# Performance work log

Measured on AMD Instinct MI355X. Metric: run time of the kernel, lower is better.

## Reference

```python
import jax, jax.numpy as jnp
import numpy as np

DIM = 128
H = 8
HD = DIM // H
NL = 6
DFF = 2048
EPS = 1e-5
S2S_STEPS = 6


def _ln(x, g, b):
    m = jnp.mean(x, -1, keepdims=True)
    v = jnp.mean(jnp.square(x - m), -1, keepdims=True)
    return (x - m) / jnp.sqrt(v + EPS) * g + b


def _lstm_step(x, h, c, wih, whh, bih, bhh):
    # torch LSTM gate order: i, f, g, o
    gates = x @ wih.T + bih + h @ whh.T + bhh
    i, f, g, o = jnp.split(gates, 4, axis=-1)
    c = jax.nn.sigmoid(f) * c + jax.nn.sigmoid(i) * jnp.tanh(g)
    h = jax.nn.sigmoid(o) * jnp.tanh(c)
    return h, c


def setup_inputs() -> dict:
    key = jax.random.key(0)
    ks = iter(jax.random.split(key, 16))
    n = lambda shape: jax.random.normal(next(ks), shape, jnp.float32) * 0.02
    inp = {
        "data": jax.random.normal(next(ks), (64, 256, 3), jnp.float32),
        "lin0_w": n((DIM, 3)), "lin0_b": jnp.zeros((DIM,), jnp.float32),
        "attn_in_w": n((NL, 3 * DIM, DIM)), "attn_in_b": jnp.zeros((NL, 3 * DIM), jnp.float32),
        "attn_out_w": n((NL, DIM, DIM)), "attn_out_b": jnp.zeros((NL, DIM), jnp.float32),
        "ln1_g": jnp.ones((NL, DIM), jnp.float32), "ln1_b": jnp.zeros((NL, DIM), jnp.float32),
        "ff_w1": n((NL, DFF, DIM)), "ff_b1": jnp.zeros((NL, DFF), jnp.float32),
        "ff_w2": n((NL, DIM, DFF)), "ff_b2": jnp.zeros((NL, DIM), jnp.float32),
        "ln2_g": jnp.ones((NL, DIM), jnp.float32), "ln2_b": jnp.zeros((NL, DIM), jnp.float32),
        "s2s_wih": n((4 * DIM, 2 * DIM)), "s2s_whh": n((4 * DIM, DIM)),
        "s2s_bih": jnp.zeros((4 * DIM,), jnp.float32), "s2s_bhh": jnp.zeros((4 * DIM,), jnp.float32),
        "mem_wih": n((4 * DIM, 2 * DIM)), "mem_whh": n((4 * DIM, DIM)),
        "mem_bih": jnp.zeros((4 * DIM,), jnp.float32), "mem_bhh": jnp.zeros((4 * DIM,), jnp.float32),
        "lin1_w": n((DIM, DIM)), "lin1_b": jnp.zeros((DIM,), jnp.float32),
        "lin3_w": n((1, DIM)), "lin3_b": jnp.zeros((1,), jnp.float32),
    }
    return inp


def reference(data, lin0_w, lin0_b, attn_in_w, attn_in_b, attn_out_w, attn_out_b,
              ln1_g, ln1_b, ff_w1, ff_b1, ff_w2, ff_b2, ln2_g, ln2_b,
              s2s_wih, s2s_whh, s2s_bih, s2s_bhh,
              mem_wih, mem_whh, mem_bih, mem_bhh,
              lin1_w, lin1_b, lin3_w, lin3_b):
    x = jax.nn.relu(data @ lin0_w.T + lin0_b)  # [S=64, B=256, D]
    S, B, _ = x.shape
    # torch TransformerEncoder with batch_first=False: attention over axis 0,
    # axis 1 is the transformer batch. Post-norm layers (norm_first=False), relu FFN.
    for l in range(NL):
        qkv = x @ attn_in_w[l].T + attn_in_b[l]
        q, k, v = jnp.split(qkv, 3, axis=-1)
        q = q.reshape(S, B, H, HD)
        k = k.reshape(S, B, H, HD)
        v = v.reshape(S, B, H, HD)
        scores = jnp.einsum('sbhd,tbhd->bhst', q, k) / np.float32(np.sqrt(HD))
        attn = jax.nn.softmax(scores, axis=-1)
        ao = jnp.einsum('bhst,tbhd->sbhd', attn, v).reshape(S, B, DIM)
        x = _ln(x + ao @ attn_out_w[l].T + attn_out_b[l], ln1_g[l], ln1_b[l])
        ff = jax.nn.relu(x @ ff_w1[l].T + ff_b1[l]) @ ff_w2[l].T + ff_b2[l]
        x = _ln(x + ff, ln2_g[l], ln2_b[l])
    # Set2Set pooling: bidxs assign segment = axis-0 index for each block of
    # num_atoms consecutive rows of flatten(out,0,1), i.e. pool over axis 1.
    q_star = jnp.zeros((S, 2 * DIM), x.dtype)
    h = jnp.zeros((S, DIM), x.dtype)
    c = jnp.zeros((S, DIM), x.dtype)
    for _ in range(S2S_STEPS):
        h, c = _lstm_step(q_star, h, c, s2s_wih, s2s_whh, s2s_bih, s2s_bhh)
        e = jnp.einsum('bnd,bd->bn', x, h)          # [S, num_atoms]
        a = jax.nn.softmax(e, axis=-1)              # segment softmax (uniform segs)
        r = jnp.einsum('bn,bnd->bd', a, x)          # segment weighted sum
        q_star = jnp.concatenate([h, r], axis=-1)   # [S, 2D]
    # memory LSTM: seq_len 1, zero initial state (states=None branch)
    hx = jnp.zeros((S, DIM), x.dtype)
    cx = jnp.zeros((S, DIM), x.dtype)
    hx, cx = _lstm_step(q_star, hx, cx, mem_wih, mem_whh, mem_bih, mem_bhh)
    o = jax.nn.relu(hx @ lin1_w.T + lin1_b)
    v_out = (o @ lin3_w.T + lin3_b)[None]  # [1, S, 1]
    return v_out, hx[None], cx[None]
```

## Files before the change

### kernel.cpp

```cpp
#include <hip/hip_runtime.h>
#include <math.h>


typedef _Float16 __attribute__((ext_vector_type(8))) f16x8;
typedef __attribute__((ext_vector_type(4))) float f32x4;
typedef _Float16 __attribute__((ext_vector_type(2))) h16x2;

__device__ __forceinline__ unsigned short f2h(float f) {
  union { _Float16 h; unsigned short s; } x; x.h = (_Float16)f; return x.s;
}
__device__ __forceinline__ float h2f(unsigned short u) {
  union { unsigned short s; _Float16 h; } x; x.s = u; return (float)x.h;
}
__device__ __forceinline__ unsigned packh(float a, float b) {
  return (unsigned)f2h(a) | ((unsigned)f2h(b) << 16);
}
__device__ __forceinline__ float hlo(unsigned u) {
  union { unsigned short s; _Float16 h; } x; x.s = (unsigned short)(u & 0xffff);
  return (float)x.h;
}
__device__ __forceinline__ float hhi(unsigned u) {
  union { unsigned short s; _Float16 h; } x; x.s = (unsigned short)(u >> 16);
  return (float)x.h;
}
__device__ __forceinline__ float fdot2u(unsigned a, unsigned b, float c) {
#if __has_builtin(__builtin_amdgcn_fdot2)
  union U { unsigned u; h16x2 h; };
  U x, y; x.u = a; y.u = b;
  return __builtin_amdgcn_fdot2(x.h, y.h, c, false);
#else
  return c + hlo(a) * hlo(b) + hhi(a) * hhi(b);
#endif
}
__device__ __forceinline__ float sigf(float x) { return 1.f / (1.f + expf(-x)); }

__device__ __forceinline__ void gl2lds16(const void* g, void* l) {
  __builtin_amdgcn_global_load_lds(
      (const __attribute__((address_space(1))) unsigned int*)g,
      (__attribute__((address_space(3))) unsigned int*)l, 16, 0, 0);
}

__global__ __launch_bounds__(256) void convw_kernel(
    const float* __restrict__ aiw, const float* __restrict__ aow,
    const float* __restrict__ w1, const float* __restrict__ w2,
    const float* __restrict__ wih, const float* __restrict__ whh,
    const float* __restrict__ mwih,
    unsigned short* __restrict__ o0, unsigned short* __restrict__ o1,
    unsigned short* __restrict__ o2, unsigned short* __restrict__ o3,
    unsigned short* __restrict__ o4, unsigned short* __restrict__ o5,
    unsigned short* __restrict__ o6) {
  int i = blockIdx.x * 256 + threadIdx.x;
  if (i < 294912) {
    o0[i] = f2h(aiw[i]);
  } else if (i < 393216) {
    int j = i - 294912; o1[j] = f2h(aow[j]);
  } else if (i < 1966080) {
    int j = i - 393216; o2[j] = f2h(w1[j]);
  } else if (i < 3538944) {
    int j = i - 1966080; o3[j] = f2h(w2[j]);
  } else if (i < 3670016) {
    int j = i - 3538944; o4[j] = f2h(wih[j]);
  } else if (i < 3735552) {
    int j = i - 3670016; o5[j] = f2h(whh[j]);
  } else {
    int j = i - 3735552; o6[j] = f2h(mwih[j]);
  }
}

__global__ __launch_bounds__(256) void lin0_kernel(
    const float* __restrict__ data, const float* __restrict__ w,
    const float* __restrict__ b, float* __restrict__ x,
    unsigned short* __restrict__ xb) {
  int i = blockIdx.x * 256 + threadIdx.x;
  int n = i >> 7, d = i & 127;
  float v = b[d] + data[n * 3 + 0] * w[d * 3 + 0]
                 + data[n * 3 + 1] * w[d * 3 + 1]
                 + data[n * 3 + 2] * w[d * 3 + 2];
  v = fmaxf(v, 0.0f);
  x[i] = v;
  xb[i] = f2h(v);
}

__global__ __launch_bounds__(512) void layer_kernel(
    const unsigned short* __restrict__ xbg,
    const unsigned short* __restrict__ wqkv, const float* __restrict__ bqkv,
    const unsigned short* __restrict__ wout, const float* __restrict__ bout,
    const float* __restrict__ ln1g, const float* __restrict__ ln1b,
    const unsigned short* __restrict__ w1, const float* __restrict__ b1,
    const unsigned short* __restrict__ w2, const float* __restrict__ b2,
    const float* __restrict__ ln2g, const float* __restrict__ ln2b,
    float* __restrict__ xio, unsigned short* __restrict__ xbo) {
  __shared__ __align__(16) unsigned short Xs[64 * 128];
  __shared__ __align__(16) unsigned short Ws[256 * 128];
  __shared__ __align__(16) unsigned short U1[128 * 128];
  __shared__ __align__(16) unsigned short U2[128 * 128];
  __shared__ __align__(16) uint4 zchunk;
  __shared__ float psum[8][64], psq[8][64];
  __shared__ float2 stats[64];

  unsigned short* Qs = U1;
  unsigned short* Ks2 = U1 + 8192;
  unsigned short* VT = U2;
  unsigned short* AOs = U2 + 8192;
  unsigned short* Hs = U2;

  int tid = threadIdx.x, w = tid >> 6, lane = tid & 63;
  int b = blockIdx.x;
  int r4 = lane >> 4, cs = lane & 15;
  int fr = lane & 15, fq = lane >> 4;

  if (tid == 0) zchunk = make_uint4(0u, 0u, 0u, 0u);

#pragma unroll
  for (int i = 0; i < 2; i++) {
    int issue = w * 2 + i;
    int row = issue * 4 + r4;
    int g = cs ^ (row & 7);
    gl2lds16(xbg + (size_t)(row * 256 + b) * 128 + g * 8,
             (char*)Xs + issue * 1024);
  }
#pragma unroll
  for (int i = 0; i < 8; i++) {
    int issue = w * 8 + i;
    int row = issue * 4 + r4;
    int g = cs ^ (row & 7);
    gl2lds16(wqkv + (size_t)row * 128 + g * 8, (char*)Ws + issue * 1024);
  }
  __syncthreads();

  f16x8 xfragA[4][4];
#pragma unroll
  for (int ks = 0; ks < 4; ks++)
#pragma unroll
    for (int mi = 0; mi < 4; mi++) {
      int row = mi * 16 + fr;
      int kq = (ks * 4 + fq) ^ (row & 7);
      xfragA[ks][mi] = *(const f16x8*)(Xs + row * 128 + kq * 8);
    }

  {
    f32x4 acc[4][2];
#pragma unroll
    for (int i = 0; i < 4; i++)
#pragma unroll
      for (int j = 0; j < 2; j++) acc[i][j] = (f32x4){0.f, 0.f, 0.f, 0.f};
#pragma unroll
    for (int ks = 0; ks < 4; ks++) {
      f16x8 bf[2];
#pragma unroll
      for (int ni = 0; ni < 2; ni++) {
        int wr = (w * 2 + ni) * 16 + fr;
        int kq = (ks * 4 + fq) ^ (wr & 7);
        bf[ni] = *(const f16x8*)(Ws + wr * 128 + kq * 8);
      }
#pragma unroll
      for (int mi = 0; mi < 4; mi++)
#pragma unroll
        for (int ni = 0; ni < 2; ni++)
          acc[mi][ni] = __builtin_amdgcn_mfma_f32_16x16x32_f16(
              xfragA[ks][mi], bf[ni], acc[mi][ni], 0, 0, 0);
    }
#pragma unroll
    for (int ni = 0; ni < 2; ni++) {
      int c = (w * 2 + ni) * 16 + fr;
      float bv = bqkv[c];
      unsigned short* dst = (c < 128) ? Qs : Ks2;
      int cc = c & 127;
#pragma unroll
      for (int mi = 0; mi < 4; mi++)
#pragma unroll
        for (int r = 0; r < 4; r++) {
          int row = mi * 16 + fq * 4 + r;
          dst[row * 128 + (((cc >> 3) ^ (row & 7)) << 3) + (cc & 7)] =
              f2h(acc[mi][ni][r] + bv);
        }
    }
  }
  __syncthreads();

#pragma unroll
  for (int i = 0; i < 4; i++) {
    int issue = w * 4 + i;
    int row = issue * 4 + r4;
    int g = cs ^ (row & 7);
    gl2lds16(wqkv + (size_t)(256 + row) * 128 + g * 8, (char*)Ws + issue * 1024);
  }
  __syncthreads();

  {
    f32x4 acc[4];
#pragma unroll
    for (int i = 0; i < 4; i++) acc[i] = (f32x4){0.f, 0.f, 0.f, 0.f};
#pragma unroll
    for (int ks = 0; ks < 4; ks++) {
      f16x8 bf;
      {
        int wr = w * 16 + fr;
        int kq = (ks * 4 + fq) ^ (wr & 7);
        bf = *(const f16x8*)(Ws + wr * 128 + kq * 8);
      }
#pragma unroll
      for (int mi = 0; mi < 4; mi++)
        acc[mi] = __builtin_amdgcn_mfma_f32_16x16x32_f16(xfragA[ks][mi], bf,
                                                         acc[mi], 0, 0, 0);
    }
    int f = w * 16 + fr;
    float bv = bqkv[256 + f];
#pragma unroll
    for (int mi = 0; mi < 4; mi++)
#pragma unroll
      for (int r = 0; r < 4; r++) {
        int srow = mi * 16 + fq * 4 + r;
        VT[f * 64 + (((srow >> 3) ^ (f & 7)) << 3) + (srow & 7)] =
            f2h(acc[mi][r] + bv);
      }
  }
  __syncthreads();

  {
    int h = w;
    unsigned short* Pb = Ws + w * 4096;
    f32x4 sc[4][4];
#pragma unroll
    for (int i = 0; i < 4; i++)
#pragma unroll
      for (int j = 0; j < 4; j++) sc[i][j] = (f32x4){0.f, 0.f, 0.f, 0.f};
    {
      f16x8 af[4], bf[4];
#pragma unroll
      for (int mi = 0; mi < 4; mi++) {
        int row = mi * 16 + fr;
        const unsigned short* pa =
            (fq < 2) ? (Qs + row * 128 + (((h * 2 + fq) ^ (row & 7)) << 3))
                     : (const unsigned short*)&zchunk;
        af[mi] = *(const f16x8*)pa;
      }
#pragma unroll
      for (int ti = 0; ti < 4; ti++) {
        int trow = ti * 16 + fr;
        const unsigned short* pb =
            (fq < 2) ? (Ks2 + trow * 128 + (((h * 2 + fq) ^ (trow & 7)) << 3))
                     : (const unsigned short*)&zchunk;
        bf[ti] = *(const f16x8*)pb;
      }
#pragma unroll
      for (int mi = 0; mi < 4; mi++)
#pragma unroll
        for (int ti = 0; ti < 4; ti++)
          sc[mi][ti] = __builtin_amdgcn_mfma_f32_16x16x32_f16(
              af[mi], bf[ti], sc[mi][ti], 0, 0, 0);
    }
#pragma unroll
    for (int mi = 0; mi < 4; mi++) {
#pragma unroll
      for (int r = 0; r < 4; r++) {
        float m = -1e30f;
#pragma unroll
        for (int ti = 0; ti < 4; ti++) m = fmaxf(m, sc[mi][ti][r]);
        m = fmaxf(m, __shfl_xor(m, 1, 64));
        m = fmaxf(m, __shfl_xor(m, 2, 64));
        m = fmaxf(m, __shfl_xor(m, 4, 64));
        m = fmaxf(m, __shfl_xor(m, 8, 64));
        m *= 0.25f;
        float ss = 0.f;
#pragma unroll
        for (int ti = 0; ti < 4; ti++) {
          float p = expf(sc[mi][ti][r] * 0.25f - m);
          sc[mi][ti][r] = p;
          ss += p;
        }
        ss += __shfl_xor(ss, 1, 64);
        ss += __shfl_xor(ss, 2, 64);
        ss += __shfl_xor(ss, 4, 64);
        ss += __shfl_xor(ss, 8, 64);
        float inv = 1.f / ss;
        int prow = mi * 16 + fq * 4 + r;
#pragma unroll
        for (int ti = 0; ti < 4; ti++) {
          int t = ti * 16 + fr;
          Pb[prow * 64 + (((t >> 3) ^ (prow & 7)) << 3) + (t & 7)] =
              f2h(sc[mi][ti][r] * inv);
        }
      }
    }
    f32x4 po[4];
#pragma unroll
    for (int i = 0; i < 4; i++) po[i] = (f32x4){0.f, 0.f, 0.f, 0.f};
#pragma unroll
    for (int ks2 = 0; ks2 < 2; ks2++) {
      f16x8 af[4], bf;
#pragma unroll
      for (int si = 0; si < 4; si++) {
        int prow = si * 16 + fr;
        int kq = (ks2 * 4 + fq) ^ (prow & 7);
        af[si] = *(const f16x8*)(Pb + prow * 64 + kq * 8);
      }
      {
        int vrow = h * 16 + fr;
        int kq = (ks2 * 4 + fq) ^ (vrow & 7);
        bf = *(const f16x8*)(VT + vrow * 64 + kq * 8);
      }
#pragma unroll
      for (int si = 0; si < 4; si++)
        po[si] = __builtin_amdgcn_mfma_f32_16x16x32_f16(af[si], bf, po[si],
                                                        0, 0, 0);
    }
#pragma unroll
    for (int si = 0; si < 4; si++)
#pragma unroll
      for (int r = 0; r < 4; r++) {
        int arow = si * 16 + fq * 4 + r;
        int c = h * 16 + fr;
        AOs[arow * 128 + (((c >> 3) ^ (arow & 7)) << 3) + (c & 7)] =
            f2h(po[si][r]);
      }
  }
  __syncthreads();

#pragma unroll
  for (int i = 0; i < 4; i++) {
    int issue = w * 4 + i;
    int row = issue * 4 + r4;
    int g = cs ^ (row & 7);
    gl2lds16(wout + (size_t)row * 128 + g * 8, (char*)Ws + issue * 1024);
  }
  __syncthreads();

  {
    f32x4 acc[4];
#pragma unroll
    for (int i = 0; i < 4; i++) acc[i] = (f32x4){0.f, 0.f, 0.f, 0.f};
#pragma unroll
    for (int ks = 0; ks < 4; ks++) {
      f16x8 af[4], bf;
#pragma unroll
      for (int si = 0; si < 4; si++) {
        int row = si * 16 + fr;
        int kq = (ks * 4 + fq) ^ (row & 7);
        af[si] = *(const f16x8*)(AOs + row * 128 + kq * 8);
      }
      {
        int wr = w * 16 + fr;
        int kq = (ks * 4 + fq) ^ (wr & 7);
        bf = *(const f16x8*)(Ws + wr * 128 + kq * 8);
      }
#pragma unroll
      for (int si = 0; si < 4; si++)
        acc[si] = __builtin_amdgcn_mfma_f32_16x16x32_f16(af[si], bf, acc[si],
                                                         0, 0, 0);
    }
    int c = w * 16 + fr;
    float bv = bout[c];
    float vv4[4][4];
    float sums[4][4], sqs[4][4];
#pragma unroll
    for (int si = 0; si < 4; si++)
#pragma unroll
      for (int r = 0; r < 4; r++) {
        int row = si * 16 + fq * 4 + r;
        float v = acc[si][r] + bv + xio[(size_t)(row * 256 + b) * 128 + c];
        vv4[si][r] = v;
        sums[si][r] = v;
        sqs[si][r] = v * v;
      }
#pragma unroll
    for (int d = 1; d < 16; d <<= 1) {
#pragma unroll
      for (int si = 0; si < 4; si++)
#pragma unroll
        for (int r = 0; r < 4; r++) {
          sums[si][r] += __shfl_xor(sums[si][r], d, 64);
          sqs[si][r] += __shfl_xor(sqs[si][r], d, 64);
        }
    }
    if (fr == 0) {
#pragma unroll
      for (int si = 0; si < 4; si++)
#pragma unroll
        for (int r = 0; r < 4; r++) {
          int row = si * 16 + fq * 4 + r;
          psum[w][row] = sums[si][r];
          psq[w][row] = sqs[si][r];
        }
    }
    __syncthreads();

#pragma unroll
    for (int i = 0; i < 4; i++) {
      int issue = w * 4 + i;
      int row = issue * 4 + r4;
      int g = cs ^ (row & 7);
      gl2lds16(w1 + (size_t)row * 128 + g * 8, (char*)Ws + issue * 1024);
      gl2lds16(w2 + (size_t)row * 2048 + g * 8, (char*)U1 + issue * 1024);
    }
    if (tid < 64) {
      float S = 0.f, Q = 0.f;
#pragma unroll
      for (int ww = 0; ww < 8; ww++) { S += psum[ww][tid]; Q += psq[ww][tid]; }
      float m = S * (1.f / 128.f);
      float var = Q * (1.f / 128.f) - m * m;
      stats[tid] = make_float2(m, rsqrtf(var + 1e-5f));
    }
    __syncthreads();
    float gl = ln1g[c], bl = ln1b[c];
#pragma unroll
    for (int si = 0; si < 4; si++)
#pragma unroll
      for (int r = 0; r < 4; r++) {
        int row = si * 16 + fq * 4 + r;
        float2 st2 = stats[row];
        float y = (vv4[si][r] - st2.x) * st2.y * gl + bl;
        Xs[row * 128 + (((c >> 3) ^ (row & 7)) << 3) + (c & 7)] = f2h(y);
      }
  }
  __syncthreads();

  f16x8 xfragF[4][4];
#pragma unroll
  for (int ks = 0; ks < 4; ks++)
#pragma unroll
    for (int mi = 0; mi < 4; mi++) {
      int row = mi * 16 + fr;
      int kq = (ks * 4 + fq) ^ (row & 7);
      xfragF[ks][mi] = *(const f16x8*)(Xs + row * 128 + kq * 8);
    }

  f32x4 acc2[4];
#pragma unroll
  for (int i = 0; i < 4; i++) acc2[i] = (f32x4){0.f, 0.f, 0.f, 0.f};

  for (int c = 0; c < 16; c++) {
    const unsigned short* W1cur = Ws + (c & 1) * 16384;
    f32x4 acc1[4];
#pragma unroll
    for (int i = 0; i < 4; i++) acc1[i] = (f32x4){0.f, 0.f, 0.f, 0.f};
#pragma unroll
    for (int ks = 0; ks < 4; ks++) {
      f16x8 bf;
      {
        int row = w * 16 + fr;
        int kq = (ks * 4 + fq) ^ (row & 7);
        bf = *(const f16x8*)(W1cur + row * 128 + kq * 8);
      }
#pragma unroll
      for (int mi = 0; mi < 4; mi++)
        acc1[mi] = __builtin_amdgcn_mfma_f32_16x16x32_f16(xfragF[ks][mi], bf,
                                                          acc1[mi], 0, 0, 0);
    }
    if (c < 15) {
#pragma unroll
      for (int i = 0; i < 4; i++) {
        int issue = w * 4 + i;
        int row = issue * 4 + r4;
        int g = cs ^ (row & 7);
        gl2lds16(w1 + (size_t)((c + 1) * 128 + row) * 128 + g * 8,
                 (char*)Ws + ((c + 1) & 1) * 32768 + issue * 1024);
      }
    }
    {
      int col = w * 16 + fr;
      float bv = b1[c * 128 + col];
#pragma unroll
      for (int mi = 0; mi < 4; mi++)
#pragma unroll
        for (int r = 0; r < 4; r++) {
          int row = mi * 16 + fq * 4 + r;
          Hs[row * 128 + (((col >> 3) ^ (row & 7)) << 3) + (col & 7)] =
              f2h(fmaxf(acc1[mi][r] + bv, 0.f));
        }
    }
    __syncthreads();

#pragma unroll
    for (int ks = 0; ks < 4; ks++) {
      f16x8 af[4], bf;
#pragma unroll
      for (int si = 0; si < 4; si++) {
        int row = si * 16 + fr;
        int kq = (ks * 4 + fq) ^ (row & 7);
        af[si] = *(const f16x8*)(Hs + row * 128 + kq * 8);
      }
      {
        int row = w * 16 + fr;
        int kq = (ks * 4 + fq) ^ (row & 7);
        bf = *(const f16x8*)(U1 + row * 128 + kq * 8);
      }
#pragma unroll
      for (int si = 0; si < 4; si++)
        acc2[si] = __builtin_amdgcn_mfma_f32_16x16x32_f16(af[si], bf, acc2[si],
                                                          0, 0, 0);
    }
    __syncthreads();
    if (c < 15) {
#pragma unroll
      for (int i = 0; i < 4; i++) {
        int issue = w * 4 + i;
        int row = issue * 4 + r4;
        int g = cs ^ (row & 7);
        gl2lds16(w2 + (size_t)row * 2048 + (c + 1) * 128 + g * 8,
                 (char*)U1 + issue * 1024);
      }
    }
  }

  {
    int c = w * 16 + fr;
    float bv = b2[c];
    float vv4[4][4];
    float sums[4][4], sqs[4][4];
#pragma unroll
    for (int si = 0; si < 4; si++)
#pragma unroll
      for (int r = 0; r < 4; r++) {
        int row = si * 16 + fq * 4 + r;
        float resid =
            h2f(Xs[row * 128 + (((c >> 3) ^ (row & 7)) << 3) + (c & 7)]);
        float v = acc2[si][r] + bv + resid;
        vv4[si][r] = v;
        sums[si][r] = v;
        sqs[si][r] = v * v;
      }
#pragma unroll
    for (int d = 1; d < 16; d <<= 1) {
#pragma unroll
      for (int si = 0; si < 4; si++)
#pragma unroll
        for (int r = 0; r < 4; r++) {
          sums[si][r] += __shfl_xor(sums[si][r], d, 64);
          sqs[si][r] += __shfl_xor(sqs[si][r], d, 64);
        }
    }
    if (fr == 0) {
#pragma unroll
      for (int si = 0; si < 4; si++)
#pragma unroll
        for (int r = 0; r < 4; r++) {
          int row = si * 16 + fq * 4 + r;
          psum[w][row] = sums[si][r];
          psq[w][row] = sqs[si][r];
        }
    }
    __syncthreads();
    if (tid < 64) {
      float S = 0.f, Q = 0.f;
#pragma unroll
      for (int ww = 0; ww < 8; ww++) { S += psum[ww][tid]; Q += psq[ww][tid]; }
      float m = S * (1.f / 128.f);
      float var = Q * (1.f / 128.f) - m * m;
      stats[tid] = make_float2(m, rsqrtf(var + 1e-5f));
    }
    __syncthreads();
    float gl = ln2g[c], bl = ln2b[c];
#pragma unroll
    for (int si = 0; si < 4; si++)
#pragma unroll
      for (int r = 0; r < 4; r++) {
        int row = si * 16 + fq * 4 + r;
        float2 st = stats[row];
        float y = (vv4[si][r] - st.x) * st.y * gl + bl;
        size_t o = (size_t)(row * 256 + b) * 128 + c;
        xio[o] = y;
        xbo[o] = f2h(y);
      }
  }
}

__global__ __launch_bounds__(512, 1) void s2s_kernel(
    const unsigned short* __restrict__ xb,
    const unsigned short* __restrict__ wihh,
    const unsigned short* __restrict__ whhh,
    const float* __restrict__ bih, const float* __restrict__ bhh,
    const unsigned short* __restrict__ mwihh,
    const float* __restrict__ mbih, const float* __restrict__ mbhh,
    const float* __restrict__ l1w, const float* __restrict__ l1b,
    const float* __restrict__ l3w, const float* __restrict__ l3b,
    float* __restrict__ out) {
  __shared__ __align__(16) unsigned xl[256 * 65];
  __shared__ __align__(16) unsigned qu[128];
  __shared__ __align__(16) float cst[128];
  __shared__ __align__(16) float gates[512];
  __shared__ __align__(16) float red[256];
  __shared__ __align__(16) float aw[256];
  int s = blockIdx.x, t = threadIdx.x, lane = t & 63, w = t >> 6;

  uint4 wreg[32], ureg[16];
  {
    const uint4* wp = (const uint4*)(wihh + (size_t)t * 256);
#pragma unroll
    for (int i = 0; i < 32; i++) wreg[i] = wp[i];
    const uint4* up = (const uint4*)(whhh + (size_t)t * 128);
#pragma unroll
    for (int i = 0; i < 16; i++) ureg[i] = up[i];
  }

  const uint4* xs4 = (const uint4*)(xb + (size_t)s * 32768);
#pragma unroll
  for (int it = 0; it < 8; it++) {
    int f = it * 512 + t;
    uint4 v = xs4[f];
    int n = f >> 4, jc = (f & 15) * 4;
    unsigned* dst = xl + n * 65 + jc;
    dst[0] = v.x; dst[1] = v.y; dst[2] = v.z; dst[3] = v.w;
  }
  if (t < 128) cst[t] = 0.f;
  __syncthreads();

  const uint4* q4 = (const uint4*)qu;
  float bsum = bih[t] + bhh[t];

  for (int step = 0; step < 6; step++) {
    if (step > 0) {
      float a0 = 0.f, a1 = 0.f, a2 = 0.f, a3 = 0.f;
#pragma unroll
      for (int i = 0; i < 16; i++) {
        uint4 qv = q4[i];
        a0 = fdot2u(wreg[i].x, qv.x, a0);
        a1 = fdot2u(wreg[i].y, qv.y, a1);
        a2 = fdot2u(wreg[i].z, qv.z, a2);
        a3 = fdot2u(wreg[i].w, qv.w, a3);
        a0 = fdot2u(ureg[i].x, qv.x, a0);
        a1 = fdot2u(ureg[i].y, qv.y, a1);
        a2 = fdot2u(ureg[i].z, qv.z, a2);
        a3 = fdot2u(ureg[i].w, qv.w, a3);
      }
#pragma unroll
      for (int i = 16; i < 32; i++) {
        uint4 qv = q4[i];
        a0 = fdot2u(wreg[i].x, qv.x, a0);
        a1 = fdot2u(wreg[i].y, qv.y, a1);
        a2 = fdot2u(wreg[i].z, qv.z, a2);
        a3 = fdot2u(wreg[i].w, qv.w, a3);
      }
      gates[t] = bsum + ((a0 + a1) + (a2 + a3));
    } else {
      gates[t] = bsum;
    }
    __syncthreads();
    if (t < 128) {
      float ig = sigf(gates[t]), fg = sigf(gates[128 + t]);
      float gg = tanhf(gates[256 + t]), og = sigf(gates[384 + t]);
      float cn = fg * cst[t] + ig * gg;
      cst[t] = cn;
      float hn = og * tanhf(cn);
      float hp = __shfl_xor(hn, 1, 64);
      if ((t & 1) == 0) qu[t >> 1] = packh(hn, hp);
    }
    __syncthreads();
    if (step > 0) {
      int n = t >> 1, p = t & 1;
      const unsigned* xr = xl + n * 65 + p * 32;
      float e0 = 0.f, e1 = 0.f;
#pragma unroll 8
      for (int i = 0; i < 32; i += 2) {
        e0 = fdot2u(xr[i], qu[p * 32 + i], e0);
        e1 = fdot2u(xr[i + 1], qu[p * 32 + i + 1], e1);
      }
      float e = e0 + e1;
      e += __shfl_xor(e, 1, 64);
      if (p == 0) red[n] = e;
      __syncthreads();
      float v0 = red[lane], v1 = red[64 + lane];
      float v2 = red[128 + lane], v3 = red[192 + lane];
      float m = fmaxf(fmaxf(v0, v1), fmaxf(v2, v3));
#pragma unroll
      for (int d = 1; d < 64; d <<= 1) m = fmaxf(m, __shfl_xor(m, d, 64));
      float p0 = expf(v0 - m), p1 = expf(v1 - m);
      float p2 = expf(v2 - m), p3 = expf(v3 - m);
      float ss = p0 + p1 + p2 + p3;
#pragma unroll
      for (int d = 1; d < 64; d <<= 1) ss += __shfl_xor(ss, d, 64);
      float Sinv = 1.f / ss;
      if (w == 0) {
        aw[lane] = p0 * Sinv; aw[64 + lane] = p1 * Sinv;
        aw[128 + lane] = p2 * Sinv; aw[192 + lane] = p3 * Sinv;
      }
    } else {
      if (t < 256) aw[t] = 1.f / 256.f;
    }
    __syncthreads();
    {
      int d = t & 127, grp = t >> 7;
      const unsigned* xc = xl + grp * 64 * 65 + (d >> 1);
      int hi = d & 1;
      const float* ap = aw + grp * 64;
      float r = 0.f;
#pragma unroll 8
      for (int n2 = 0; n2 < 64; n2++) {
        unsigned u = xc[n2 * 65];
        r += ap[n2] * (hi ? hhi(u) : hlo(u));
      }
      gates[t] = r;
    }
    __syncthreads();
    if (t < 128) {
      float rd = gates[t] + gates[128 + t] + gates[256 + t] + gates[384 + t];
      float rp = __shfl_xor(rd, 1, 64);
      if ((t & 1) == 0) qu[64 + (t >> 1)] = packh(rd, rp);
    }
    __syncthreads();
  }
  {
    float a0 = 0.f, a1 = 0.f, a2 = 0.f, a3 = 0.f;
    const uint4* mp = (const uint4*)(mwihh + (size_t)t * 256);
#pragma unroll 8
    for (int i = 0; i < 32; i++) {
      uint4 wv = mp[i], qv = q4[i];
      a0 = fdot2u(wv.x, qv.x, a0);
      a1 = fdot2u(wv.y, qv.y, a1);
      a2 = fdot2u(wv.z, qv.z, a2);
      a3 = fdot2u(wv.w, qv.w, a3);
    }
    gates[t] = mbih[t] + mbhh[t] + ((a0 + a1) + (a2 + a3));
  }
  __syncthreads();
  if (t < 128) {
    float ig = sigf(gates[t]);
    float gg = tanhf(gates[256 + t]);
    float og = sigf(gates[384 + t]);
    float cx = ig * gg;
    float hx = og * tanhf(cx);
    cst[t] = hx;
    out[64 + s * 128 + t] = hx;
    out[64 + 8192 + s * 128 + t] = cx;
  }
  __syncthreads();
  if (t < 128) {
    float acc = l1b[t];
    const float4* w4 = (const float4*)(l1w + (size_t)t * 128);
    const float4* h4 = (const float4*)cst;
#pragma unroll 8
    for (int k = 0; k < 32; k++) {
      float4 a = w4[k], b = h4[k];
      acc += a.x * b.x + a.y * b.y + a.z * b.z + a.w * b.w;
    }
    red[t] = fmaxf(acc, 0.f) * l3w[t];
  } else if (t < 256) {
    red[t] = 0.f;
  }
  __syncthreads();
  for (int off = 128; off; off >>= 1) {
    if (t < off) red[t] += red[t + off];
    __syncthreads();
  }
  if (t == 0) out[s] = red[0] + l3b[0];
}

extern "C" void kernel_launch(void* const* d_in, const int* in_sizes, int n_in,
                              void* d_out, int out_size, void* d_ws,
                              size_t ws_size, hipStream_t stream) {
  const float* data       = (const float*)d_in[0];
  const float* lin0_w     = (const float*)d_in[1];
  const float* lin0_b     = (const float*)d_in[2];
  const float* attn_in_w  = (const float*)d_in[3];
  const float* attn_in_b  = (const float*)d_in[4];
  const float* attn_out_w = (const float*)d_in[5];
  const float* attn_out_b = (const float*)d_in[6];
  const float* ln1_g      = (const float*)d_in[7];
  const float* ln1_b      = (const float*)d_in[8];
  const float* ff_w1      = (const float*)d_in[9];
  const float* ff_b1      = (const float*)d_in[10];
  const float* ff_w2      = (const float*)d_in[11];
  const float* ff_b2      = (const float*)d_in[12];
  const float* ln2_g      = (const float*)d_in[13];
  const float* ln2_b      = (const float*)d_in[14];
  const float* s2s_wih    = (const float*)d_in[15];
  const float* s2s_whh    = (const float*)d_in[16];
  const float* s2s_bih    = (const float*)d_in[17];
  const float* s2s_bhh    = (const float*)d_in[18];
  const float* mem_wih    = (const float*)d_in[19];
  const float* mem_bih    = (const float*)d_in[21];
  const float* mem_bhh    = (const float*)d_in[22];
  const float* lin1_w     = (const float*)d_in[23];
  const float* lin1_b     = (const float*)d_in[24];
  const float* lin3_w     = (const float*)d_in[25];
  const float* lin3_b     = (const float*)d_in[26];
  float* out = (float*)d_out;

  char* p = (char*)d_ws;
  float* x = (float*)p;                      p += (size_t)16384 * 128 * 4;
  unsigned short* xb = (unsigned short*)p;   p += (size_t)16384 * 128 * 2;
  unsigned short* wqkv = (unsigned short*)p; p += (size_t)294912 * 2;
  unsigned short* wout = (unsigned short*)p; p += (size_t)98304 * 2;
  unsigned short* w1h = (unsigned short*)p;  p += (size_t)1572864 * 2;
  unsigned short* w2h = (unsigned short*)p;  p += (size_t)1572864 * 2;
  unsigned short* wihh = (unsigned short*)p; p += (size_t)131072 * 2;
  unsigned short* whhh = (unsigned short*)p; p += (size_t)65536 * 2;
  unsigned short* mwihh = (unsigned short*)p; p += (size_t)131072 * 2;

  convw_kernel<<<15104, 256, 0, stream>>>(
      attn_in_w, attn_out_w, ff_w1, ff_w2, s2s_wih, s2s_whh, mem_wih,
      wqkv, wout, w1h, w2h, wihh, whhh, mwihh);
  lin0_kernel<<<8192, 256, 0, stream>>>(data, lin0_w, lin0_b, x, xb);

  for (int l = 0; l < 6; l++) {
    layer_kernel<<<256, 512, 0, stream>>>(
        xb, wqkv + (size_t)l * 49152, attn_in_b + l * 384,
        wout + (size_t)l * 16384, attn_out_b + l * 128,
        ln1_g + l * 128, ln1_b + l * 128,
        w1h + (size_t)l * 262144, ff_b1 + l * 2048,
        w2h + (size_t)l * 262144, ff_b2 + l * 128,
        ln2_g + l * 128, ln2_b + l * 128, x, xb);
  }

  s2s_kernel<<<64, 512, 0, stream>>>(
      xb, wihh, whhh, s2s_bih, s2s_bhh,
      mwihh, mem_bih, mem_bhh, lin1_w, lin1_b, lin3_w, lin3_b, out);
}
```

Before: 483.8 us.

## Pre-swizzle weights into MFMA fragment order and load B operands directly to registers

The weight conversion kernel now writes the attention, output and FFN weights permuted into the per-lane MFMA B-fragment order. The layer kernel then loads each wave's B fragments straight from global memory into registers, dropping the global-to-LDS staging of weights and several barriers. The FFN hidden tile is double-buffered in LDS so one barrier per chunk is removed. The cost is that every block re-reads weights from global/L2 with per-lane 16-byte loads, and those loads are no longer prefetched a stage ahead, so their latency can show up directly.

```diff
diff --git a/kernel.cpp b/kernel.cpp
--- a/kernel.cpp
+++ b/kernel.cpp
@@ -51,13 +51,28 @@
     unsigned short* __restrict__ o6) {
   int i = blockIdx.x * 256 + threadIdx.x;
   if (i < 294912) {
-    o0[i] = f2h(aiw[i]);
+    int l = i / 49152, o = i % 49152;
+    int j = o & 7, fr = (o >> 3) & 15, fq = (o >> 7) & 3, ks = (o >> 9) & 3,
+        rb = o >> 11;
+    o0[i] = f2h(aiw[l * 49152 + (rb * 16 + fr) * 128 + ks * 32 + fq * 8 + j]);
   } else if (i < 393216) {
-    int j = i - 294912; o1[j] = f2h(aow[j]);
+    int ii = i - 294912;
+    int l = ii / 16384, o = ii % 16384;
+    int j = o & 7, fr = (o >> 3) & 15, fq = (o >> 7) & 3, ks = (o >> 9) & 3,
+        rb = o >> 11;
+    o1[ii] = f2h(aow[l * 16384 + (rb * 16 + fr) * 128 + ks * 32 + fq * 8 + j]);
   } else if (i < 1966080) {
-    int j = i - 393216; o2[j] = f2h(w1[j]);
+    int ii = i - 393216;
+    int l = ii >> 18, o = ii & 262143;
+    int j = o & 7, fr = (o >> 3) & 15, fq = (o >> 7) & 3, ks = (o >> 9) & 3,
+        rb = o >> 11;
+    o2[ii] = f2h(w1[l * 262144 + (rb * 16 + fr) * 128 + ks * 32 + fq * 8 + j]);
   } else if (i < 3538944) {
-    int j = i - 1966080; o3[j] = f2h(w2[j]);
+    int ii = i - 1966080;
+    int l = ii >> 18, o = ii & 262143;
+    int j = o & 7, fr = (o >> 3) & 15, fq = (o >> 7) & 3, ks = (o >> 9) & 63,
+        rb = o >> 15;
+    o3[ii] = f2h(w2[l * 262144 + (rb * 16 + fr) * 2048 + ks * 32 + fq * 8 + j]);
   } else if (i < 3670016) {
     int j = i - 3538944; o4[j] = f2h(wih[j]);
   } else if (i < 3735552) {
@@ -102,7 +117,6 @@
   unsigned short* Ks2 = U1 + 8192;
   unsigned short* VT = U2;
   unsigned short* AOs = U2 + 8192;
-  unsigned short* Hs = U2;
 
   int tid = threadIdx.x, w = tid >> 6, lane = tid & 63;
   int b = blockIdx.x;
@@ -119,13 +133,13 @@
     gl2lds16(xbg + (size_t)(row * 256 + b) * 128 + g * 8,
              (char*)Xs + issue * 1024);
   }
-#pragma unroll
-  for (int i = 0; i < 8; i++) {
-    int issue = w * 8 + i;
-    int row = issue * 4 + r4;
-    int g = cs ^ (row & 7);
-    gl2lds16(wqkv + (size_t)row * 128 + g * 8, (char*)Ws + issue * 1024);
-  }
+  f16x8 bqk[4][2];
+#pragma unroll
+  for (int ks = 0; ks < 4; ks++)
+#pragma unroll
+    for (int ni = 0; ni < 2; ni++)
+      bqk[ks][ni] = *(const f16x8*)(wqkv + (w * 2 + ni) * 2048 + ks * 512 +
+                                    fq * 128 + fr * 8);
   __syncthreads();
 
   f16x8 xfragA[4][4];
@@ -145,21 +159,13 @@
 #pragma unroll
       for (int j = 0; j < 2; j++) acc[i][j] = (f32x4){0.f, 0.f, 0.f, 0.f};
 #pragma unroll
-    for (int ks = 0; ks < 4; ks++) {
-      f16x8 bf[2];
-#pragma unroll
-      for (int ni = 0; ni < 2; ni++) {
-        int wr = (w * 2 + ni) * 16 + fr;
-        int kq = (ks * 4 + fq) ^ (wr & 7);
-        bf[ni] = *(const f16x8*)(Ws + wr * 128 + kq * 8);
-      }
+    for (int ks = 0; ks < 4; ks++)
 #pragma unroll
       for (int mi = 0; mi < 4; mi++)
 #pragma unroll
         for (int ni = 0; ni < 2; ni++)
           acc[mi][ni] = __builtin_amdgcn_mfma_f32_16x16x32_f16(
-              xfragA[ks][mi], bf[ni], acc[mi][ni], 0, 0, 0);
-    }
+              xfragA[ks][mi], bqk[ks][ni], acc[mi][ni], 0, 0, 0);
 #pragma unroll
     for (int ni = 0; ni < 2; ni++) {
       int c = (w * 2 + ni) * 16 + fr;
@@ -176,15 +182,11 @@
         }
     }
   }
-  __syncthreads();
-
-#pragma unroll
-  for (int i = 0; i < 4; i++) {
-    int issue = w * 4 + i;
-    int row = issue * 4 + r4;
-    int g = cs ^ (row & 7);
-    gl2lds16(wqkv + (size_t)(256 + row) * 128 + g * 8, (char*)Ws + issue * 1024);
-  }
+  f16x8 bv4[4];
+#pragma unroll
+  for (int ks = 0; ks < 4; ks++)
+    bv4[ks] = *(const f16x8*)(wqkv + (16 + w) * 2048 + ks * 512 + fq * 128 +
+                              fr * 8);
   __syncthreads();
 
   {
@@ -192,18 +194,12 @@
 #pragma unroll
     for (int i = 0; i < 4; i++) acc[i] = (f32x4){0.f, 0.f, 0.f, 0.f};
 #pragma unroll
-    for (int ks = 0; ks < 4; ks++) {
-      f16x8 bf;
-      {
-        int wr = w * 16 + fr;
-        int kq = (ks * 4 + fq) ^ (wr & 7);
-        bf = *(const f16x8*)(Ws + wr * 128 + kq * 8);
-      }
+    for (int ks = 0; ks < 4; ks++)
 #pragma unroll
       for (int mi = 0; mi < 4; mi++)
-        acc[mi] = __builtin_amdgcn_mfma_f32_16x16x32_f16(xfragA[ks][mi], bf,
-                                                         acc[mi], 0, 0, 0);
-    }
+        acc[mi] = __builtin_amdgcn_mfma_f32_16x16x32_f16(xfragA[ks][mi],
+                                                         bv4[ks], acc[mi],
+                                                         0, 0, 0);
     int f = w * 16 + fr;
     float bv = bqkv[256 + f];
 #pragma unroll
@@ -315,15 +311,10 @@
             f2h(po[si][r]);
       }
   }
-  __syncthreads();
-
-#pragma unroll
-  for (int i = 0; i < 4; i++) {
-    int issue = w * 4 + i;
-    int row = issue * 4 + r4;
-    int g = cs ^ (row & 7);
-    gl2lds16(wout + (size_t)row * 128 + g * 8, (char*)Ws + issue * 1024);
-  }
+  f16x8 bwo[4];
+#pragma unroll
+  for (int ks = 0; ks < 4; ks++)
+    bwo[ks] = *(const f16x8*)(wout + w * 2048 + ks * 512 + fq * 128 + fr * 8);
   __syncthreads();
 
   {
@@ -332,22 +323,17 @@
     for (int i = 0; i < 4; i++) acc[i] = (f32x4){0.f, 0.f, 0.f, 0.f};
 #pragma unroll
     for (int ks = 0; ks < 4; ks++) {
-      f16x8 af[4], bf;
+      f16x8 af[4];
 #pragma unroll
       for (int si = 0; si < 4; si++) {
         int row = si * 16 + fr;
         int kq = (ks * 4 + fq) ^ (row & 7);
         af[si] = *(const f16x8*)(AOs + row * 128 + kq * 8);
       }
-      {
-        int wr = w * 16 + fr;
-        int kq = (ks * 4 + fq) ^ (wr & 7);
-        bf = *(const f16x8*)(Ws + wr * 128 + kq * 8);
-      }
 #pragma unroll
       for (int si = 0; si < 4; si++)
-        acc[si] = __builtin_amdgcn_mfma_f32_16x16x32_f16(af[si], bf, acc[si],
-                                                         0, 0, 0);
+        acc[si] = __builtin_amdgcn_mfma_f32_16x16x32_f16(af[si], bwo[ks],
+                                                         acc[si], 0, 0, 0);
     }
     int c = w * 16 + fr;
     float bv = bout[c];
@@ -384,15 +370,6 @@
         }
     }
     __syncthreads();
-
-#pragma unroll
-    for (int i = 0; i < 4; i++) {
-      int issue = w * 4 + i;
-      int row = issue * 4 + r4;
-      int g = cs ^ (row & 7);
-      gl2lds16(w1 + (size_t)row * 128 + g * 8, (char*)Ws + issue * 1024);
-      gl2lds16(w2 + (size_t)row * 2048 + g * 8, (char*)U1 + issue * 1024);
-    }
     if (tid < 64) {
       float S = 0.f, Q = 0.f;
 #pragma unroll
@@ -430,33 +407,26 @@
   for (int i = 0; i < 4; i++) acc2[i] = (f32x4){0.f, 0.f, 0.f, 0.f};
 
   for (int c = 0; c < 16; c++) {
-    const unsigned short* W1cur = Ws + (c & 1) * 16384;
+    unsigned short* Hcur = Ws + (c & 1) * 8192;
+    f16x8 bw1[4], bw2[4];
+#pragma unroll
+    for (int ks = 0; ks < 4; ks++)
+      bw1[ks] = *(const f16x8*)(w1 + (size_t)(c * 8 + w) * 2048 + ks * 512 +
+                                fq * 128 + fr * 8);
+#pragma unroll
+    for (int ks = 0; ks < 4; ks++)
+      bw2[ks] = *(const f16x8*)(w2 + (size_t)w * 32768 + (c * 4 + ks) * 512 +
+                                fq * 128 + fr * 8);
     f32x4 acc1[4];
 #pragma unroll
     for (int i = 0; i < 4; i++) acc1[i] = (f32x4){0.f, 0.f, 0.f, 0.f};
 #pragma unroll
-    for (int ks = 0; ks < 4; ks++) {
-      f16x8 bf;
-      {
-        int row = w * 16 + fr;
-        int kq = (ks * 4 + fq) ^ (row & 7);
-        bf = *(const f16x8*)(W1cur + row * 128 + kq * 8);
-      }
+    for (int ks = 0; ks < 4; ks++)
 #pragma unroll
       for (int mi = 0; mi < 4; mi++)
-        acc1[mi] = __builtin_amdgcn_mfma_f32_16x16x32_f16(xfragF[ks][mi], bf,
-                                                          acc1[mi], 0, 0, 0);
-    }
-    if (c < 15) {
-#pragma unroll
-      for (int i = 0; i < 4; i++) {
-        int issue = w * 4 + i;
-        int row = issue * 4 + r4;
-        int g = cs ^ (row & 7);
-        gl2lds16(w1 + (size_t)((c + 1) * 128 + row) * 128 + g * 8,
-                 (char*)Ws + ((c + 1) & 1) * 32768 + issue * 1024);
-      }
-    }
+        acc1[mi] = __builtin_amdgcn_mfma_f32_16x16x32_f16(xfragF[ks][mi],
+                                                          bw1[ks], acc1[mi],
+                                                          0, 0, 0);
     {
       int col = w * 16 + fr;
       float bv = b1[c * 128 + col];
@@ -465,41 +435,24 @@
 #pragma unroll
         for (int r = 0; r < 4; r++) {
           int row = mi * 16 + fq * 4 + r;
-          Hs[row * 128 + (((col >> 3) ^ (row & 7)) << 3) + (col & 7)] =
+          Hcur[row * 128 + (((col >> 3) ^ (row & 7)) << 3) + (col & 7)] =
               f2h(fmaxf(acc1[mi][r] + bv, 0.f));
         }
     }
     __syncthreads();
-
 #pragma unroll
     for (int ks = 0; ks < 4; ks++) {
-      f16x8 af[4], bf;
+      f16x8 af[4];
 #pragma unroll
       for (int si = 0; si < 4; si++) {
         int row = si * 16 + fr;
         int kq = (ks * 4 + fq) ^ (row & 7);
-        af[si] = *(const f16x8*)(Hs + row * 128 + kq * 8);
-      }
-      {
-        int row = w * 16 + fr;
-        int kq = (ks * 4 + fq) ^ (row & 7);
-        bf = *(const f16x8*)(U1 + row * 128 + kq * 8);
+        af[si] = *(const f16x8*)(Hcur + row * 128 + kq * 8);
       }
 #pragma unroll
       for (int si = 0; si < 4; si++)
-        acc2[si] = __builtin_amdgcn_mfma_f32_16x16x32_f16(af[si], bf, acc2[si],
-                                                          0, 0, 0);
-    }
-    __syncthreads();
-    if (c < 15) {
-#pragma unroll
-      for (int i = 0; i < 4; i++) {
-        int issue = w * 4 + i;
-        int row = issue * 4 + r4;
-        int g = cs ^ (row & 7);
-        gl2lds16(w2 + (size_t)row * 2048 + (c + 1) * 128 + g * 8,
-                 (char*)U1 + issue * 1024);
-      }
+        acc2[si] = __builtin_amdgcn_mfma_f32_16x16x32_f16(af[si], bw2[ks],
+                                                          acc2[si], 0, 0, 0);
     }
   }
 
```

After: 459.4 us. 1.05x faster.
